# Performance work log

Measured on AMD Instinct MI355X. Metric: run time of the kernel, lower is better.

## Reference

```python
import jax, jax.numpy as jnp
import numpy as np

H = 128      # hidden_dim
D = 2        # data_dim
T = 20       # obs_len
B = 16384    # batch
PRED = 30    # pred_len
LN_EPS = 1e-5


def _lstm_cell(x, h, c, Wih, Whh, bih, bhh):
    # torch gate order: i, f, g, o
    gates = x @ Wih.T + h @ Whh.T + bih + bhh
    i, f, g, o = jnp.split(gates, 4, axis=-1)
    c = jax.nn.sigmoid(f) * c + jax.nn.sigmoid(i) * jnp.tanh(g)
    h = jax.nn.sigmoid(o) * jnp.tanh(c)
    return h, c


def _encode(seq, Wih, Whh, bih, bhh):
    # seq: [T, B, D]; return final (h, c)
    b = seq.shape[1]
    h0 = jnp.zeros((b, H), seq.dtype)
    def step(carry, x):
        h, c = _lstm_cell(x, carry[0], carry[1], Wih, Whh, bih, bhh)
        return (h, c), None
    (h, c), _ = jax.lax.scan(step, (h0, h0), seq)
    return h, c


def _layernorm(x, g, b):
    m = jnp.mean(x, axis=-1, keepdims=True)
    v = jnp.var(x, axis=-1, keepdims=True)
    return (x - m) * jax.lax.rsqrt(v + LN_EPS) * g + b


def setup_inputs() -> dict:
    key = jax.random.key(0)
    ks = jax.random.split(key, 20)
    s_in = 1.0 / np.sqrt(H)  # torch default LSTM init scale
    def W(k, shape):
        return jax.random.normal(k, shape, jnp.float32) * s_in
    return {
        "pos": jax.random.normal(ks[0], (T, B, D), jnp.float32),
        "speed": jax.random.normal(ks[1], (T, B, D), jnp.float32),
        "Wih_pe": W(ks[2], (4 * H, D)), "Whh_pe": W(ks[3], (4 * H, H)),
        "bih_pe": W(ks[4], (4 * H,)), "bhh_pe": W(ks[5], (4 * H,)),
        "Wih_se": W(ks[6], (4 * H, D)), "Whh_se": W(ks[7], (4 * H, H)),
        "bih_se": W(ks[8], (4 * H,)), "bhh_se": W(ks[9], (4 * H,)),
        "ln_g": jnp.ones((H,), jnp.float32), "ln_b": jnp.zeros((H,), jnp.float32),
        "Wih_sd": W(ks[10], (4 * H, D)), "Whh_sd": W(ks[11], (4 * H, H)),
        "bih_sd": W(ks[12], (4 * H,)), "bhh_sd": W(ks[13], (4 * H,)),
        "Wih_pd": W(ks[14], (4 * H, D)), "Whh_pd": W(ks[15], (4 * H, H)),
        "bih_pd": W(ks[16], (4 * H,)), "bhh_pd": W(ks[17], (4 * H,)),
        "Wfc": W(ks[18], (D, H)), "bfc": jnp.zeros((D,), jnp.float32),
    }


def reference(pos, speed, Wih_pe, Whh_pe, bih_pe, bhh_pe,
              Wih_se, Whh_se, bih_se, bhh_se, ln_g, ln_b,
              Wih_sd, Whh_sd, bih_sd, bhh_sd,
              Wih_pd, Whh_pd, bih_pd, bhh_pd, Wfc, bfc):
    hpo, cpo = _encode(pos, Wih_pe, Whh_pe, bih_pe, bhh_pe)
    hpo = _layernorm(hpo, ln_g, ln_b)
    cpo = _layernorm(cpo, ln_g, ln_b)
    hsp, csp = _encode(speed, Wih_se, Whh_se, bih_se, bhh_se)
    hsp = _layernorm(hsp, ln_g, ln_b)
    csp = _layernorm(csp, ln_g, ln_b)

    # concat_features=False path
    hds, cds = hpo + hsp, cpo + csp
    curr_speed, curr_pos = speed[-1], pos[-1]

    def step(carry, _):
        hds, cds, hpo, cpo, cs, cp = carry
        hds, cds = _lstm_cell(cs, hds, cds, Wih_sd, Whh_sd, bih_sd, bhh_sd)
        cs = hds @ Wfc.T + bfc
        hpo, cpo = _lstm_cell(cp, hpo, cpo, Wih_pd, Whh_pd, bih_pd, bhh_pd)
        cp = hpo @ Wfc.T + bfc
        return (hds, cds, hpo, cpo, cs, cp), (cp, cs)

    _, (pos_out, speed_out) = jax.lax.scan(
        step, (hds, cds, hpo, cpo, curr_speed, curr_pos), None, length=PRED)
    return pos_out, speed_out  # each [PRED, B, D]
```

## Files before the change

kernel.cpp:

```cpp
#include <hip/hip_runtime.h>

#define H 128
#define D 2
#define T_OBS 20
#define BATCH 16384
#define PRED 30
#define M 32
#define NTH 512
#define HP 136
#define FP 132
#define LN_EPS 1e-5f

typedef __attribute__((ext_vector_type(8))) _Float16 half8_t;
typedef __attribute__((ext_vector_type(4))) float float4_t;

__device__ __forceinline__ float fast_rcp(float x){ return __builtin_amdgcn_rcpf(x); }
__device__ __forceinline__ float sig_f(float x){ return fast_rcp(1.f + __expf(-x)); }
__device__ __forceinline__ float tanh_f(float x){ return 1.f - 2.f*fast_rcp(__expf(2.f*x)+1.f); }

struct PhaseConsts {
  half8_t bw[4][4];
  float bs[4], w0[4], w1[4];
};

__device__ __forceinline__ void load_phase(PhaseConsts& P, const float* __restrict__ Whh,
                                           const float* __restrict__ Wih,
                                           const float* __restrict__ bih,
                                           const float* __restrict__ bhh,
                                           int wv, int l15, int q){
#pragma unroll
  for(int g=0; g<4; g++){
    const int n = g*H + 16*wv + l15;
    P.bs[g] = bih[n] + bhh[n];
    P.w0[g] = Wih[n*D + 0];
    P.w1[g] = Wih[n*D + 1];
#pragma unroll
    for(int ks=0; ks<4; ks++){
      const float* p = Whh + (size_t)n*H + ks*32 + q*8;
      float4 a = *(const float4*)p;
      float4 b = *(const float4*)(p+4);
      half8_t f;
      f[0]=(_Float16)a.x; f[1]=(_Float16)a.y; f[2]=(_Float16)a.z; f[3]=(_Float16)a.w;
      f[4]=(_Float16)b.x; f[5]=(_Float16)b.y; f[6]=(_Float16)b.z; f[7]=(_Float16)b.w;
      P.bw[g][ks] = f;
    }
  }
}

__device__ __forceinline__ void load_phase_dec(PhaseConsts& P, const float* __restrict__ Whh,
                                               const float* __restrict__ Wih,
                                               const float* __restrict__ bih,
                                               const float* __restrict__ bhh,
                                               const float* __restrict__ Wfc,
                                               const float* __restrict__ bfc,
                                               int wv, int l15, int q){
#pragma unroll
  for(int g=0; g<4; g++){
    const int n = g*H + 16*wv + l15;
    const float wi0 = Wih[n*D + 0];
    const float wi1 = Wih[n*D + 1];
    P.bs[g] = bih[n] + bhh[n] + wi0*bfc[0] + wi1*bfc[1];
    P.w0[g] = wi0;
    P.w1[g] = wi1;
#pragma unroll
    for(int ks=0; ks<4; ks++){
      const float* p  = Whh + (size_t)n*H + ks*32 + q*8;
      const float* f0 = Wfc + 0*H + ks*32 + q*8;
      const float* f1 = Wfc + 1*H + ks*32 + q*8;
      half8_t f;
#pragma unroll
      for(int j=0;j<8;j++){
        f[j] = (_Float16)(p[j] + wi0*f0[j] + wi1*f1[j]);
      }
      P.bw[g][ks] = f;
    }
  }
}

template<bool HASX>
__device__ __forceinline__ void cell_step(_Float16 (*hsh)[M][HP], int cur,
                                          const float* __restrict__ xsrc,
                                          const PhaseConsts& P, float (&c)[2][4],
                                          int wv, int l15, int q){
  float4_t acc[2][4];
  if constexpr (HASX){
#pragma unroll
    for(int mh=0; mh<2; mh++){
      float x0[4], x1[4];
#pragma unroll
      for(int r=0; r<4; r++){
        x0[r] = xsrc[(mh*16 + 4*q+r)*2 + 0];
        x1[r] = xsrc[(mh*16 + 4*q+r)*2 + 1];
      }
#pragma unroll
      for(int g=0; g<4; g++)
#pragma unroll
        for(int r=0; r<4; r++)
          acc[mh][g][r] = fmaf(P.w1[g], x1[r], fmaf(P.w0[g], x0[r], P.bs[g]));
    }
  } else {
#pragma unroll
    for(int mh=0; mh<2; mh++)
#pragma unroll
      for(int g=0; g<4; g++)
#pragma unroll
        for(int r=0; r<4; r++)
          acc[mh][g][r] = P.bs[g];
  }

#pragma unroll
  for(int ks=0; ks<4; ks++){
#pragma unroll
    for(int mh=0; mh<2; mh++){
      const half8_t a = *(const half8_t*)&hsh[cur][mh*16 + l15][ks*32 + q*8];
#pragma unroll
      for(int g=0; g<4; g++){
        acc[mh][g] = __builtin_amdgcn_mfma_f32_16x16x32_f16(a, P.bw[g][ks], acc[mh][g], 0,0,0);
      }
    }
  }
  const int nxt = cur ^ 1;
  const int u = 16*wv + l15;
#pragma unroll
  for(int mh=0; mh<2; mh++){
#pragma unroll
    for(int r=0; r<4; r++){
      const float iv = sig_f(acc[mh][0][r]);
      const float fv = sig_f(acc[mh][1][r]);
      const float gv = tanh_f(acc[mh][2][r]);
      const float ov = sig_f(acc[mh][3][r]);
      const float cc = fmaf(fv, c[mh][r], iv*gv);
      c[mh][r] = cc;
      const float hv = ov * tanh_f(cc);
      const int m = mh*16 + 4*q + r;
      hsh[nxt][m][u] = (_Float16)hv;
    }
  }
  __syncthreads();
}

__device__ __forceinline__ void layernorm32(const float (*src)[FP], float (*dst)[FP],
                                            const float* __restrict__ g,
                                            const float* __restrict__ b, int tid){
  const int m = tid >> 4, sub = tid & 15;
  float v[8];
  float s = 0.f, s2 = 0.f;
#pragma unroll
  for(int j=0;j<8;j++){ v[j] = src[m][sub*8+j]; s += v[j]; s2 = fmaf(v[j], v[j], s2); }
#pragma unroll
  for(int msk=1; msk<16; msk<<=1){ s += __shfl_xor(s, msk, 64); s2 += __shfl_xor(s2, msk, 64); }
  const float mean = s * (1.f/H);
  const float var  = s2 * (1.f/H) - mean*mean;
  const float inv  = rsqrtf(var + LN_EPS);
#pragma unroll
  for(int j=0;j<8;j++){
    const int u = sub*8+j;
    dst[m][u] = fmaf((v[j]-mean)*inv, g[u], b[u]);
  }
}

__device__ __forceinline__ void fc_out(const _Float16 (*hb)[HP], const float (*wfc)[H],
                                       const float* __restrict__ bfcs,
                                       float* __restrict__ gout, int row0, int tid){
  const int m = tid >> 4, d = (tid >> 3) & 1, ch = tid & 7;
  const _Float16* hp = &hb[m][ch*16];
  float s = 0.f;
#pragma unroll
  for(int j=0;j<16;j++) s = fmaf((float)hp[j], wfc[d][ch*16+j], s);
  s += __shfl_xor(s, 1, 64); s += __shfl_xor(s, 2, 64); s += __shfl_xor(s, 4, 64);
  if(ch == 0){
    gout[(size_t)(row0+m)*D + d] = s + bfcs[d];
  }
}

__device__ __forceinline__ void fc_delta(const _Float16 (*hb)[HP], const float (*wfc)[H],
                                         const float* __restrict__ bfcs,
                                         const float* __restrict__ xlast,
                                         float (*xb)[D], int tid){
  const int m = tid >> 4, d = (tid >> 3) & 1, ch = tid & 7;
  const _Float16* hp = &hb[m][ch*16];
  float s = 0.f;
#pragma unroll
  for(int j=0;j<16;j++) s = fmaf((float)hp[j], wfc[d][ch*16+j], s);
  s += __shfl_xor(s, 1, 64); s += __shfl_xor(s, 2, 64); s += __shfl_xor(s, 4, 64);
  if(ch == 0){
    xb[m][d] = xlast[m*D + d] - (s + bfcs[d]);
  }
}

__global__ __launch_bounds__(NTH, 2) void traj_kernel(
    const float* __restrict__ pos, const float* __restrict__ speed,
    const float* __restrict__ Wih_pe, const float* __restrict__ Whh_pe,
    const float* __restrict__ bih_pe, const float* __restrict__ bhh_pe,
    const float* __restrict__ Wih_se, const float* __restrict__ Whh_se,
    const float* __restrict__ bih_se, const float* __restrict__ bhh_se,
    const float* __restrict__ ln_g, const float* __restrict__ ln_b,
    const float* __restrict__ Wih_sd, const float* __restrict__ Whh_sd,
    const float* __restrict__ bih_sd, const float* __restrict__ bhh_sd,
    const float* __restrict__ Wih_pd, const float* __restrict__ Whh_pd,
    const float* __restrict__ bih_pd, const float* __restrict__ bhh_pd,
    const float* __restrict__ Wfc, const float* __restrict__ bfc,
    float* __restrict__ out)
{
  __shared__ __align__(16) _Float16 hsh[2][M][HP];
  __shared__ float tmpf[M][FP];
  __shared__ float hpoN[M][FP];
  __shared__ float cpoN[M][FP];
  __shared__ float seqx[2][T_OBS][M][D];
  __shared__ float xbuf[M][D];
  __shared__ float wfcs[D][H];
  __shared__ float bfcs[2];

  const int tid  = threadIdx.x;
  const int lane = tid & 63;
  const int wv   = tid >> 6;
  const int q    = lane >> 4;
  const int l15  = lane & 15;
  const int row0 = blockIdx.x * M;
  const int u    = 16*wv + l15;

  for(int idx = tid; idx < 2*T_OBS*M*D; idx += NTH){
    const int chain = idx / (T_OBS*M*D);
    const int rem   = idx % (T_OBS*M*D);
    const int t = rem / (M*D), e = rem % (M*D);
    const float* src = chain ? speed : pos;
    seqx[chain][t][e>>1][e&1] = src[(size_t)t*BATCH*D + row0*D + e];
  }
  if(tid < D*H) wfcs[tid>>7][tid&127] = Wfc[tid];
  if(tid < 2)   bfcs[tid] = bfc[tid];
  { int* hz = (int*)&hsh[0][0][0];
    for(int idx = tid; idx < M*HP/2; idx += NTH) hz[idx] = 0; }

  PhaseConsts P;
  float c[2][4];
  load_phase(P, Whh_pe, Wih_pe, bih_pe, bhh_pe, wv, l15, q);
#pragma unroll
  for(int mh=0;mh<2;mh++)
#pragma unroll
    for(int r=0;r<4;r++) c[mh][r] = 0.f;
  __syncthreads();

  int cur = 0;
  for(int t=0; t<T_OBS; t++){ cell_step<true>(hsh, cur, &seqx[0][t][0][0], P, c, wv, l15, q); cur ^= 1; }
  for(int idx=tid; idx<M*H; idx+=NTH){
    const int m = idx>>7, uu = idx&127;
    tmpf[m][uu] = (float)hsh[cur][m][uu];
  }
  __syncthreads();
  layernorm32(tmpf, hpoN, ln_g, ln_b, tid);
  __syncthreads();
#pragma unroll
  for(int mh=0;mh<2;mh++)
#pragma unroll
    for(int r=0;r<4;r++) tmpf[mh*16 + 4*q+r][u] = c[mh][r];
  __syncthreads();
  layernorm32(tmpf, cpoN, ln_g, ln_b, tid);
  __syncthreads();

  load_phase(P, Whh_se, Wih_se, bih_se, bhh_se, wv, l15, q);
#pragma unroll
  for(int mh=0;mh<2;mh++)
#pragma unroll
    for(int r=0;r<4;r++) c[mh][r] = 0.f;
  for(int idx=tid; idx<M*H; idx+=NTH){
    const int m = idx>>7, uu = idx&127;
    hsh[0][m][uu] = (_Float16)0.f;
  }
  cur = 0;
  __syncthreads();
  for(int t=0; t<T_OBS; t++){ cell_step<true>(hsh, cur, &seqx[1][t][0][0], P, c, wv, l15, q); cur ^= 1; }
  for(int idx=tid; idx<M*H; idx+=NTH){
    const int m = idx>>7, uu = idx&127;
    tmpf[m][uu] = (float)hsh[cur][m][uu];
  }
  __syncthreads();
  layernorm32(tmpf, tmpf, ln_g, ln_b, tid);
  __syncthreads();
  for(int idx=tid; idx<M*H; idx+=NTH){
    const int m = idx>>7, uu = idx&127;
    hsh[0][m][uu] = (_Float16)(tmpf[m][uu] + hpoN[m][uu]);
  }
  __syncthreads();
#pragma unroll
  for(int mh=0;mh<2;mh++)
#pragma unroll
    for(int r=0;r<4;r++) tmpf[mh*16 + 4*q+r][u] = c[mh][r];
  __syncthreads();
  layernorm32(tmpf, tmpf, ln_g, ln_b, tid);
  __syncthreads();
#pragma unroll
  for(int mh=0;mh<2;mh++)
#pragma unroll
    for(int r=0;r<4;r++) c[mh][r] = tmpf[mh*16 + 4*q+r][u] + cpoN[mh*16 + 4*q+r][u];

  load_phase_dec(P, Whh_sd, Wih_sd, bih_sd, bhh_sd, Wfc, bfc, wv, l15, q);
  fc_delta(hsh[0], wfcs, bfcs, &seqx[1][T_OBS-1][0][0], xbuf, tid);
  __syncthreads();

  float* spd_out = out + (size_t)PRED*BATCH*D;
  cur = 0;
  cell_step<true>(hsh, cur, &xbuf[0][0], P, c, wv, l15, q);
  fc_out(hsh[cur^1], wfcs, bfcs, spd_out, row0, tid);
  cur ^= 1;
  for(int t=1; t<PRED; t++){
    cell_step<false>(hsh, cur, nullptr, P, c, wv, l15, q);
    fc_out(hsh[cur^1], wfcs, bfcs, spd_out + (size_t)t*BATCH*D, row0, tid);
    cur ^= 1;
  }
  __syncthreads();

  for(int idx=tid; idx<M*H; idx+=NTH){
    const int m = idx>>7, uu = idx&127;
    hsh[0][m][uu] = (_Float16)hpoN[m][uu];
  }
#pragma unroll
  for(int mh=0;mh<2;mh++)
#pragma unroll
    for(int r=0;r<4;r++) c[mh][r] = cpoN[mh*16 + 4*q+r][u];
  load_phase_dec(P, Whh_pd, Wih_pd, bih_pd, bhh_pd, Wfc, bfc, wv, l15, q);
  __syncthreads();
  fc_delta(hsh[0], wfcs, bfcs, &seqx[0][T_OBS-1][0][0], xbuf, tid);
  __syncthreads();

  cur = 0;
  cell_step<true>(hsh, cur, &xbuf[0][0], P, c, wv, l15, q);
  fc_out(hsh[cur^1], wfcs, bfcs, out, row0, tid);
  cur ^= 1;
  for(int t=1; t<PRED; t++){
    cell_step<false>(hsh, cur, nullptr, P, c, wv, l15, q);
    fc_out(hsh[cur^1], wfcs, bfcs, out + (size_t)t*BATCH*D, row0, tid);
    cur ^= 1;
  }
}

extern "C" void kernel_launch(void* const* d_in, const int* in_sizes, int n_in,
                              void* d_out, int out_size, void* d_ws, size_t ws_size,
                              hipStream_t stream)
{
  const float* pos    = (const float*)d_in[0];
  const float* speed  = (const float*)d_in[1];
  const float* Wih_pe = (const float*)d_in[2];
  const float* Whh_pe = (const float*)d_in[3];
  const float* bih_pe = (const float*)d_in[4];
  const float* bhh_pe = (const float*)d_in[5];
  const float* Wih_se = (const float*)d_in[6];
  const float* Whh_se = (const float*)d_in[7];
  const float* bih_se = (const float*)d_in[8];
  const float* bhh_se = (const float*)d_in[9];
  const float* ln_g   = (const float*)d_in[10];
  const float* ln_b   = (const float*)d_in[11];
  const float* Wih_sd = (const float*)d_in[12];
  const float* Whh_sd = (const float*)d_in[13];
  const float* bih_sd = (const float*)d_in[14];
  const float* bhh_sd = (const float*)d_in[15];
  const float* Wih_pd = (const float*)d_in[16];
  const float* Whh_pd = (const float*)d_in[17];
  const float* bih_pd = (const float*)d_in[18];
  const float* bhh_pd = (const float*)d_in[19];
  const float* Wfc    = (const float*)d_in[20];
  const float* bfc    = (const float*)d_in[21];

  traj_kernel<<<BATCH/M, NTH, 0, stream>>>(
      pos, speed, Wih_pe, Whh_pe, bih_pe, bhh_pe,
      Wih_se, Whh_se, bih_se, bhh_se, ln_g, ln_b,
      Wih_sd, Whh_sd, bih_sd, bhh_sd, Wih_pd, Whh_pd, bih_pd, bhh_pd,
      Wfc, bfc, (float*)d_out);
}
```

Before: 547.5 us.

## Split batch rows across two wave groups with 1024-thread blocks

Doubles the block to 1024 threads. Each group of 8 waves now handles one 16-row half of the 32-row tile instead of one wave handling both halves. This halves the MFMA and gate work per wave on each recurrent step, shortening the serial critical path between barriers. LayerNorm and FC helpers are gated to the first 512 threads. The cost is a heavier __syncthreads across 16 waves, half the threads idle during FC, and the loss of the 2-blocks-per-CU launch bound, which may cut occupancy.

```diff
diff --git a/kernel.cpp b/kernel.cpp
--- a/kernel.cpp
+++ b/kernel.cpp
@@ -6,7 +6,7 @@
 #define BATCH 16384
 #define PRED 30
 #define M 32
-#define NTH 512
+#define NTH 1024
 #define HP 136
 #define FP 132
 #define LN_EPS 1e-5f
@@ -27,10 +27,10 @@
                                            const float* __restrict__ Wih,
                                            const float* __restrict__ bih,
                                            const float* __restrict__ bhh,
-                                           int wv, int l15, int q){
+                                           int wvu, int l15, int q){
 #pragma unroll
   for(int g=0; g<4; g++){
-    const int n = g*H + 16*wv + l15;
+    const int n = g*H + 16*wvu + l15;
     P.bs[g] = bih[n] + bhh[n];
     P.w0[g] = Wih[n*D + 0];
     P.w1[g] = Wih[n*D + 1];
@@ -53,10 +53,10 @@
                                                const float* __restrict__ bhh,
                                                const float* __restrict__ Wfc,
                                                const float* __restrict__ bfc,
-                                               int wv, int l15, int q){
+                                               int wvu, int l15, int q){
 #pragma unroll
   for(int g=0; g<4; g++){
-    const int n = g*H + 16*wv + l15;
+    const int n = g*H + 16*wvu + l15;
     const float wi0 = Wih[n*D + 0];
     const float wi1 = Wih[n*D + 1];
     P.bs[g] = bih[n] + bhh[n] + wi0*bfc[0] + wi1*bfc[1];
@@ -80,61 +80,48 @@
 template<bool HASX>
 __device__ __forceinline__ void cell_step(_Float16 (*hsh)[M][HP], int cur,
                                           const float* __restrict__ xsrc,
-                                          const PhaseConsts& P, float (&c)[2][4],
-                                          int wv, int l15, int q){
-  float4_t acc[2][4];
+                                          const PhaseConsts& P, float (&c)[4],
+                                          int mrow0, int arow, int u, int l15, int q){
+  float4_t acc[4];
   if constexpr (HASX){
-#pragma unroll
-    for(int mh=0; mh<2; mh++){
-      float x0[4], x1[4];
-#pragma unroll
-      for(int r=0; r<4; r++){
-        x0[r] = xsrc[(mh*16 + 4*q+r)*2 + 0];
-        x1[r] = xsrc[(mh*16 + 4*q+r)*2 + 1];
-      }
-#pragma unroll
-      for(int g=0; g<4; g++)
-#pragma unroll
-        for(int r=0; r<4; r++)
-          acc[mh][g][r] = fmaf(P.w1[g], x1[r], fmaf(P.w0[g], x0[r], P.bs[g]));
+    float x0[4], x1[4];
+#pragma unroll
+    for(int r=0; r<4; r++){
+      x0[r] = xsrc[(mrow0 + 4*q+r)*2 + 0];
+      x1[r] = xsrc[(mrow0 + 4*q+r)*2 + 1];
     }
+#pragma unroll
+    for(int g=0; g<4; g++)
+#pragma unroll
+      for(int r=0; r<4; r++)
+        acc[g][r] = fmaf(P.w1[g], x1[r], fmaf(P.w0[g], x0[r], P.bs[g]));
   } else {
 #pragma unroll
-    for(int mh=0; mh<2; mh++)
-#pragma unroll
-      for(int g=0; g<4; g++)
-#pragma unroll
-        for(int r=0; r<4; r++)
-          acc[mh][g][r] = P.bs[g];
+    for(int g=0; g<4; g++)
+#pragma unroll
+      for(int r=0; r<4; r++)
+        acc[g][r] = P.bs[g];
   }
 
 #pragma unroll
   for(int ks=0; ks<4; ks++){
-#pragma unroll
-    for(int mh=0; mh<2; mh++){
-      const half8_t a = *(const half8_t*)&hsh[cur][mh*16 + l15][ks*32 + q*8];
-#pragma unroll
-      for(int g=0; g<4; g++){
-        acc[mh][g] = __builtin_amdgcn_mfma_f32_16x16x32_f16(a, P.bw[g][ks], acc[mh][g], 0,0,0);
-      }
+    const half8_t a = *(const half8_t*)&hsh[cur][arow][ks*32 + q*8];
+#pragma unroll
+    for(int g=0; g<4; g++){
+      acc[g] = __builtin_amdgcn_mfma_f32_16x16x32_f16(a, P.bw[g][ks], acc[g], 0,0,0);
     }
   }
   const int nxt = cur ^ 1;
-  const int u = 16*wv + l15;
-#pragma unroll
-  for(int mh=0; mh<2; mh++){
-#pragma unroll
-    for(int r=0; r<4; r++){
-      const float iv = sig_f(acc[mh][0][r]);
-      const float fv = sig_f(acc[mh][1][r]);
-      const float gv = tanh_f(acc[mh][2][r]);
-      const float ov = sig_f(acc[mh][3][r]);
-      const float cc = fmaf(fv, c[mh][r], iv*gv);
-      c[mh][r] = cc;
-      const float hv = ov * tanh_f(cc);
-      const int m = mh*16 + 4*q + r;
-      hsh[nxt][m][u] = (_Float16)hv;
-    }
+#pragma unroll
+  for(int r=0; r<4; r++){
+    const float iv = sig_f(acc[0][r]);
+    const float fv = sig_f(acc[1][r]);
+    const float gv = tanh_f(acc[2][r]);
+    const float ov = sig_f(acc[3][r]);
+    const float cc = fmaf(fv, c[r], iv*gv);
+    c[r] = cc;
+    const float hv = ov * tanh_f(cc);
+    hsh[nxt][mrow0 + 4*q + r][u] = (_Float16)hv;
   }
   __syncthreads();
 }
@@ -142,6 +129,7 @@
 __device__ __forceinline__ void layernorm32(const float (*src)[FP], float (*dst)[FP],
                                             const float* __restrict__ g,
                                             const float* __restrict__ b, int tid){
+  if(tid >= 512) return;
   const int m = tid >> 4, sub = tid & 15;
   float v[8];
   float s = 0.f, s2 = 0.f;
@@ -162,6 +150,7 @@
 __device__ __forceinline__ void fc_out(const _Float16 (*hb)[HP], const float (*wfc)[H],
                                        const float* __restrict__ bfcs,
                                        float* __restrict__ gout, int row0, int tid){
+  if(tid >= 512) return;
   const int m = tid >> 4, d = (tid >> 3) & 1, ch = tid & 7;
   const _Float16* hp = &hb[m][ch*16];
   float s = 0.f;
@@ -177,6 +166,7 @@
                                          const float* __restrict__ bfcs,
                                          const float* __restrict__ xlast,
                                          float (*xb)[D], int tid){
+  if(tid >= 512) return;
   const int m = tid >> 4, d = (tid >> 3) & 1, ch = tid & 7;
   const _Float16* hp = &hb[m][ch*16];
   float s = 0.f;
@@ -188,7 +178,7 @@
   }
 }
 
-__global__ __launch_bounds__(NTH, 2) void traj_kernel(
+__global__ __launch_bounds__(NTH) void traj_kernel(
     const float* __restrict__ pos, const float* __restrict__ speed,
     const float* __restrict__ Wih_pe, const float* __restrict__ Whh_pe,
     const float* __restrict__ bih_pe, const float* __restrict__ bhh_pe,
@@ -214,10 +204,14 @@
   const int tid  = threadIdx.x;
   const int lane = tid & 63;
   const int wv   = tid >> 6;
+  const int wvu  = wv & 7;
+  const int mh   = wv >> 3;
   const int q    = lane >> 4;
   const int l15  = lane & 15;
   const int row0 = blockIdx.x * M;
-  const int u    = 16*wv + l15;
+  const int u    = 16*wvu + l15;
+  const int mrow0= mh*16;
+  const int arow = mrow0 + l15;
 
   for(int idx = tid; idx < 2*T_OBS*M*D; idx += NTH){
     const int chain = idx / (T_OBS*M*D);
@@ -232,16 +226,14 @@
     for(int idx = tid; idx < M*HP/2; idx += NTH) hz[idx] = 0; }
 
   PhaseConsts P;
-  float c[2][4];
-  load_phase(P, Whh_pe, Wih_pe, bih_pe, bhh_pe, wv, l15, q);
-#pragma unroll
-  for(int mh=0;mh<2;mh++)
-#pragma unroll
-    for(int r=0;r<4;r++) c[mh][r] = 0.f;
+  float c[4];
+  load_phase(P, Whh_pe, Wih_pe, bih_pe, bhh_pe, wvu, l15, q);
+#pragma unroll
+  for(int r=0;r<4;r++) c[r] = 0.f;
   __syncthreads();
 
   int cur = 0;
-  for(int t=0; t<T_OBS; t++){ cell_step<true>(hsh, cur, &seqx[0][t][0][0], P, c, wv, l15, q); cur ^= 1; }
+  for(int t=0; t<T_OBS; t++){ cell_step<true>(hsh, cur, &seqx[0][t][0][0], P, c, mrow0, arow, u, l15, q); cur ^= 1; }
   for(int idx=tid; idx<M*H; idx+=NTH){
     const int m = idx>>7, uu = idx&127;
     tmpf[m][uu] = (float)hsh[cur][m][uu];
@@ -250,25 +242,21 @@
   layernorm32(tmpf, hpoN, ln_g, ln_b, tid);
   __syncthreads();
 #pragma unroll
-  for(int mh=0;mh<2;mh++)
-#pragma unroll
-    for(int r=0;r<4;r++) tmpf[mh*16 + 4*q+r][u] = c[mh][r];
+  for(int r=0;r<4;r++) tmpf[mrow0 + 4*q+r][u] = c[r];
   __syncthreads();
   layernorm32(tmpf, cpoN, ln_g, ln_b, tid);
   __syncthreads();
 
-  load_phase(P, Whh_se, Wih_se, bih_se, bhh_se, wv, l15, q);
-#pragma unroll
-  for(int mh=0;mh<2;mh++)
-#pragma unroll
-    for(int r=0;r<4;r++) c[mh][r] = 0.f;
+  load_phase(P, Whh_se, Wih_se, bih_se, bhh_se, wvu, l15, q);
+#pragma unroll
+  for(int r=0;r<4;r++) c[r] = 0.f;
   for(int idx=tid; idx<M*H; idx+=NTH){
     const int m = idx>>7, uu = idx&127;
     hsh[0][m][uu] = (_Float16)0.f;
   }
   cur = 0;
   __syncthreads();
-  for(int t=0; t<T_OBS; t++){ cell_step<true>(hsh, cur, &seqx[1][t][0][0], P, c, wv, l15, q); cur ^= 1; }
+  for(int t=0; t<T_OBS; t++){ cell_step<true>(hsh, cur, &seqx[1][t][0][0], P, c, mrow0, arow, u, l15, q); cur ^= 1; }
   for(int idx=tid; idx<M*H; idx+=NTH){
     const int m = idx>>7, uu = idx&127;
     tmpf[m][uu] = (float)hsh[cur][m][uu];
@@ -282,28 +270,24 @@
   }
   __syncthreads();
 #pragma unroll
-  for(int mh=0;mh<2;mh++)
-#pragma unroll
-    for(int r=0;r<4;r++) tmpf[mh*16 + 4*q+r][u] = c[mh][r];
+  for(int r=0;r<4;r++) tmpf[mrow0 + 4*q+r][u] = c[r];
   __syncthreads();
   layernorm32(tmpf, tmpf, ln_g, ln_b, tid);
   __syncthreads();
 #pragma unroll
-  for(int mh=0;mh<2;mh++)
-#pragma unroll
-    for(int r=0;r<4;r++) c[mh][r] = tmpf[mh*16 + 4*q+r][u] + cpoN[mh*16 + 4*q+r][u];
-
-  load_phase_dec(P, Whh_sd, Wih_sd, bih_sd, bhh_sd, Wfc, bfc, wv, l15, q);
+  for(int r=0;r<4;r++) c[r] = tmpf[mrow0 + 4*q+r][u] + cpoN[mrow0 + 4*q+r][u];
+
+  load_phase_dec(P, Whh_sd, Wih_sd, bih_sd, bhh_sd, Wfc, bfc, wvu, l15, q);
   fc_delta(hsh[0], wfcs, bfcs, &seqx[1][T_OBS-1][0][0], xbuf, tid);
   __syncthreads();
 
   float* spd_out = out + (size_t)PRED*BATCH*D;
   cur = 0;
-  cell_step<true>(hsh, cur, &xbuf[0][0], P, c, wv, l15, q);
+  cell_step<true>(hsh, cur, &xbuf[0][0], P, c, mrow0, arow, u, l15, q);
   fc_out(hsh[cur^1], wfcs, bfcs, spd_out, row0, tid);
   cur ^= 1;
   for(int t=1; t<PRED; t++){
-    cell_step<false>(hsh, cur, nullptr, P, c, wv, l15, q);
+    cell_step<false>(hsh, cur, nullptr, P, c, mrow0, arow, u, l15, q);
     fc_out(hsh[cur^1], wfcs, bfcs, spd_out + (size_t)t*BATCH*D, row0, tid);
     cur ^= 1;
   }
@@ -314,20 +298,18 @@
     hsh[0][m][uu] = (_Float16)hpoN[m][uu];
   }
 #pragma unroll
-  for(int mh=0;mh<2;mh++)
-#pragma unroll
-    for(int r=0;r<4;r++) c[mh][r] = cpoN[mh*16 + 4*q+r][u];
-  load_phase_dec(P, Whh_pd, Wih_pd, bih_pd, bhh_pd, Wfc, bfc, wv, l15, q);
+  for(int r=0;r<4;r++) c[r] = cpoN[mrow0 + 4*q+r][u];
+  load_phase_dec(P, Whh_pd, Wih_pd, bih_pd, bhh_pd, Wfc, bfc, wvu, l15, q);
   __syncthreads();
   fc_delta(hsh[0], wfcs, bfcs, &seqx[0][T_OBS-1][0][0], xbuf, tid);
   __syncthreads();
 
   cur = 0;
-  cell_step<true>(hsh, cur, &xbuf[0][0], P, c, wv, l15, q);
+  cell_step<true>(hsh, cur, &xbuf[0][0], P, c, mrow0, arow, u, l15, q);
   fc_out(hsh[cur^1], wfcs, bfcs, out, row0, tid);
   cur ^= 1;
   for(int t=1; t<PRED; t++){
-    cell_step<false>(hsh, cur, nullptr, P, c, wv, l15, q);
+    cell_step<false>(hsh, cur, nullptr, P, c, mrow0, arow, u, l15, q);
     fc_out(hsh[cur^1], wfcs, bfcs, out + (size_t)t*BATCH*D, row0, tid);
     cur ^= 1;
   }
```

After: 0.9998 ms. 82.6% more time.

## Interleave the two independent LSTM chains in one fused dual-cell step

Applied to the files above, without the earlier changes.

The pos and speed encoders run together in one loop, and so do the two decoders, rather than one after the other. Each step issues MFMAs for both chains between barriers, which halves the number of sequential steps and __syncthreads, and gives the scheduler independent work to hide MFMA and transcendental latency. The cost is double the register state (two PhaseConsts with fp16 weight fragments plus two accumulator sets) and double the shared h buffer, which risks spills or lower occupancy under launch_bounds(512,2). Several expressions are also rewritten as fmaf.

```diff
diff --git a/kernel.cpp b/kernel.cpp
--- a/kernel.cpp
+++ b/kernel.cpp
@@ -16,7 +16,7 @@
 
 __device__ __forceinline__ float fast_rcp(float x){ return __builtin_amdgcn_rcpf(x); }
 __device__ __forceinline__ float sig_f(float x){ return fast_rcp(1.f + __expf(-x)); }
-__device__ __forceinline__ float tanh_f(float x){ return 1.f - 2.f*fast_rcp(__expf(2.f*x)+1.f); }
+__device__ __forceinline__ float tanh_f(float x){ return fmaf(-2.f, fast_rcp(__expf(2.f*x)+1.f), 1.f); }
 
 struct PhaseConsts {
   half8_t bw[4][4];
@@ -59,7 +59,7 @@
     const int n = g*H + 16*wv + l15;
     const float wi0 = Wih[n*D + 0];
     const float wi1 = Wih[n*D + 1];
-    P.bs[g] = bih[n] + bhh[n] + wi0*bfc[0] + wi1*bfc[1];
+    P.bs[g] = fmaf(wi1, bfc[1], fmaf(wi0, bfc[0], bih[n] + bhh[n]));
     P.w0[g] = wi0;
     P.w1[g] = wi1;
 #pragma unroll
@@ -70,7 +70,7 @@
       half8_t f;
 #pragma unroll
       for(int j=0;j<8;j++){
-        f[j] = (_Float16)(p[j] + wi0*f0[j] + wi1*f1[j]);
+        f[j] = (_Float16)fmaf(wi1, f1[j], fmaf(wi0, f0[j], p[j]));
       }
       P.bw[g][ks] = f;
     }
@@ -78,25 +78,41 @@
 }
 
 template<bool HASX>
-__device__ __forceinline__ void cell_step(_Float16 (*hsh)[M][HP], int cur,
-                                          const float* __restrict__ xsrc,
-                                          const PhaseConsts& P, float (&c)[2][4],
+__device__ __forceinline__ void cell_dual(_Float16 (*hsh)[2][M][HP], int cur,
+                                          const float* __restrict__ xs0,
+                                          const float* __restrict__ xs1,
+                                          const PhaseConsts& Pa, const PhaseConsts& Pb,
+                                          float (&ca)[2][4], float (&cb)[2][4],
                                           int wv, int l15, int q){
-  float4_t acc[2][4];
+  float4_t aa[2][4], ab[2][4];
   if constexpr (HASX){
 #pragma unroll
     for(int mh=0; mh<2; mh++){
       float x0[4], x1[4];
 #pragma unroll
       for(int r=0; r<4; r++){
-        x0[r] = xsrc[(mh*16 + 4*q+r)*2 + 0];
-        x1[r] = xsrc[(mh*16 + 4*q+r)*2 + 1];
+        x0[r] = xs0[(mh*16 + 4*q+r)*2 + 0];
+        x1[r] = xs0[(mh*16 + 4*q+r)*2 + 1];
       }
 #pragma unroll
       for(int g=0; g<4; g++)
 #pragma unroll
         for(int r=0; r<4; r++)
-          acc[mh][g][r] = fmaf(P.w1[g], x1[r], fmaf(P.w0[g], x0[r], P.bs[g]));
+          aa[mh][g][r] = fmaf(Pa.w1[g], x1[r], fmaf(Pa.w0[g], x0[r], Pa.bs[g]));
+    }
+#pragma unroll
+    for(int mh=0; mh<2; mh++){
+      float x0[4], x1[4];
+#pragma unroll
+      for(int r=0; r<4; r++){
+        x0[r] = xs1[(mh*16 + 4*q+r)*2 + 0];
+        x1[r] = xs1[(mh*16 + 4*q+r)*2 + 1];
+      }
+#pragma unroll
+      for(int g=0; g<4; g++)
+#pragma unroll
+        for(int r=0; r<4; r++)
+          ab[mh][g][r] = fmaf(Pb.w1[g], x1[r], fmaf(Pb.w0[g], x0[r], Pb.bs[g]));
     }
   } else {
 #pragma unroll
@@ -104,19 +120,24 @@
 #pragma unroll
       for(int g=0; g<4; g++)
 #pragma unroll
-        for(int r=0; r<4; r++)
-          acc[mh][g][r] = P.bs[g];
+        for(int r=0; r<4; r++){
+          aa[mh][g][r] = Pa.bs[g];
+          ab[mh][g][r] = Pb.bs[g];
+        }
   }
 
 #pragma unroll
   for(int ks=0; ks<4; ks++){
 #pragma unroll
     for(int mh=0; mh<2; mh++){
-      const half8_t a = *(const half8_t*)&hsh[cur][mh*16 + l15][ks*32 + q*8];
-#pragma unroll
-      for(int g=0; g<4; g++){
-        acc[mh][g] = __builtin_amdgcn_mfma_f32_16x16x32_f16(a, P.bw[g][ks], acc[mh][g], 0,0,0);
-      }
+      const half8_t h0 = *(const half8_t*)&hsh[cur][0][mh*16 + l15][ks*32 + q*8];
+#pragma unroll
+      for(int g=0; g<4; g++)
+        aa[mh][g] = __builtin_amdgcn_mfma_f32_16x16x32_f16(h0, Pa.bw[g][ks], aa[mh][g], 0,0,0);
+      const half8_t h1 = *(const half8_t*)&hsh[cur][1][mh*16 + l15][ks*32 + q*8];
+#pragma unroll
+      for(int g=0; g<4; g++)
+        ab[mh][g] = __builtin_amdgcn_mfma_f32_16x16x32_f16(h1, Pb.bw[g][ks], ab[mh][g], 0,0,0);
     }
   }
   const int nxt = cur ^ 1;
@@ -125,15 +146,25 @@
   for(int mh=0; mh<2; mh++){
 #pragma unroll
     for(int r=0; r<4; r++){
-      const float iv = sig_f(acc[mh][0][r]);
-      const float fv = sig_f(acc[mh][1][r]);
-      const float gv = tanh_f(acc[mh][2][r]);
-      const float ov = sig_f(acc[mh][3][r]);
-      const float cc = fmaf(fv, c[mh][r], iv*gv);
-      c[mh][r] = cc;
-      const float hv = ov * tanh_f(cc);
       const int m = mh*16 + 4*q + r;
-      hsh[nxt][m][u] = (_Float16)hv;
+      {
+        const float iv = sig_f(aa[mh][0][r]);
+        const float fv = sig_f(aa[mh][1][r]);
+        const float gv = tanh_f(aa[mh][2][r]);
+        const float ov = sig_f(aa[mh][3][r]);
+        const float cc = fmaf(fv, ca[mh][r], iv*gv);
+        ca[mh][r] = cc;
+        hsh[nxt][0][m][u] = (_Float16)(ov * tanh_f(cc));
+      }
+      {
+        const float iv = sig_f(ab[mh][0][r]);
+        const float fv = sig_f(ab[mh][1][r]);
+        const float gv = tanh_f(ab[mh][2][r]);
+        const float ov = sig_f(ab[mh][3][r]);
+        const float cc = fmaf(fv, cb[mh][r], iv*gv);
+        cb[mh][r] = cc;
+        hsh[nxt][1][m][u] = (_Float16)(ov * tanh_f(cc));
+      }
     }
   }
   __syncthreads();
@@ -150,7 +181,7 @@
 #pragma unroll
   for(int msk=1; msk<16; msk<<=1){ s += __shfl_xor(s, msk, 64); s2 += __shfl_xor(s2, msk, 64); }
   const float mean = s * (1.f/H);
-  const float var  = s2 * (1.f/H) - mean*mean;
+  const float var  = fmaf(-mean, mean, s2 * (1.f/H));
   const float inv  = rsqrtf(var + LN_EPS);
 #pragma unroll
   for(int j=0;j<8;j++){
@@ -159,32 +190,42 @@
   }
 }
 
-__device__ __forceinline__ void fc_out(const _Float16 (*hb)[HP], const float (*wfc)[H],
-                                       const float* __restrict__ bfcs,
-                                       float* __restrict__ gout, int row0, int tid){
-  const int m = tid >> 4, d = (tid >> 3) & 1, ch = tid & 7;
-  const _Float16* hp = &hb[m][ch*16];
-  float s = 0.f;
-#pragma unroll
-  for(int j=0;j<16;j++) s = fmaf((float)hp[j], wfc[d][ch*16+j], s);
-  s += __shfl_xor(s, 1, 64); s += __shfl_xor(s, 2, 64); s += __shfl_xor(s, 4, 64);
-  if(ch == 0){
-    gout[(size_t)(row0+m)*D + d] = s + bfcs[d];
-  }
-}
-
-__device__ __forceinline__ void fc_delta(const _Float16 (*hb)[HP], const float (*wfc)[H],
-                                         const float* __restrict__ bfcs,
-                                         const float* __restrict__ xlast,
-                                         float (*xb)[D], int tid){
-  const int m = tid >> 4, d = (tid >> 3) & 1, ch = tid & 7;
-  const _Float16* hp = &hb[m][ch*16];
-  float s = 0.f;
-#pragma unroll
-  for(int j=0;j<16;j++) s = fmaf((float)hp[j], wfc[d][ch*16+j], s);
-  s += __shfl_xor(s, 1, 64); s += __shfl_xor(s, 2, 64); s += __shfl_xor(s, 4, 64);
-  if(ch == 0){
-    xb[m][d] = xlast[m*D + d] - (s + bfcs[d]);
+__device__ __forceinline__ void fc_out_dual(const _Float16 (*hb)[M][HP], const float (*wfc)[H],
+                                            const float* __restrict__ bfcs,
+                                            float* __restrict__ g0, float* __restrict__ g1,
+                                            int row0, int tid){
+  const int m = tid >> 4, d = (tid >> 3) & 1, cn = tid & 7;
+#pragma unroll
+  for(int ch=0; ch<2; ch++){
+    const _Float16* hp = &hb[ch][m][cn*16];
+    float s = 0.f;
+#pragma unroll
+    for(int j=0;j<16;j++) s = fmaf((float)hp[j], wfc[d][cn*16+j], s);
+    s += __shfl_xor(s, 1, 64); s += __shfl_xor(s, 2, 64); s += __shfl_xor(s, 4, 64);
+    if(cn == 0){
+      float* g = ch ? g1 : g0;
+      g[(size_t)(row0+m)*D + d] = s + bfcs[d];
+    }
+  }
+}
+
+__device__ __forceinline__ void fc_delta_dual(const _Float16 (*hb)[M][HP], const float (*wfc)[H],
+                                              const float* __restrict__ bfcs,
+                                              const float* __restrict__ xl0,
+                                              const float* __restrict__ xl1,
+                                              float (*xb)[M][D], int tid){
+  const int m = tid >> 4, d = (tid >> 3) & 1, cn = tid & 7;
+#pragma unroll
+  for(int ch=0; ch<2; ch++){
+    const _Float16* hp = &hb[ch][m][cn*16];
+    float s = 0.f;
+#pragma unroll
+    for(int j=0;j<16;j++) s = fmaf((float)hp[j], wfc[d][cn*16+j], s);
+    s += __shfl_xor(s, 1, 64); s += __shfl_xor(s, 2, 64); s += __shfl_xor(s, 4, 64);
+    if(cn == 0){
+      const float* xl = ch ? xl1 : xl0;
+      xb[ch][m][d] = xl[m*D + d] - (s + bfcs[d]);
+    }
   }
 }
 
@@ -202,12 +243,12 @@
     const float* __restrict__ Wfc, const float* __restrict__ bfc,
     float* __restrict__ out)
 {
-  __shared__ __align__(16) _Float16 hsh[2][M][HP];
+  __shared__ __align__(16) _Float16 hsh[2][2][M][HP];
   __shared__ float tmpf[M][FP];
   __shared__ float hpoN[M][FP];
   __shared__ float cpoN[M][FP];
   __shared__ float seqx[2][T_OBS][M][D];
-  __shared__ float xbuf[M][D];
+  __shared__ float xbuf[2][M][D];
   __shared__ float wfcs[D][H];
   __shared__ float bfcs[2];
 
@@ -228,107 +269,81 @@
   }
   if(tid < D*H) wfcs[tid>>7][tid&127] = Wfc[tid];
   if(tid < 2)   bfcs[tid] = bfc[tid];
-  { int* hz = (int*)&hsh[0][0][0];
-    for(int idx = tid; idx < M*HP/2; idx += NTH) hz[idx] = 0; }
-
-  PhaseConsts P;
-  float c[2][4];
-  load_phase(P, Whh_pe, Wih_pe, bih_pe, bhh_pe, wv, l15, q);
+  { int* hz = (int*)&hsh[0][0][0][0];
+    for(int idx = tid; idx < M*HP; idx += NTH) hz[idx] = 0; }
+
+  PhaseConsts Pa, Pb;
+  float ca[2][4], cb[2][4];
+  load_phase(Pa, Whh_pe, Wih_pe, bih_pe, bhh_pe, wv, l15, q);
+  load_phase(Pb, Whh_se, Wih_se, bih_se, bhh_se, wv, l15, q);
 #pragma unroll
   for(int mh=0;mh<2;mh++)
 #pragma unroll
-    for(int r=0;r<4;r++) c[mh][r] = 0.f;
+    for(int r=0;r<4;r++){ ca[mh][r] = 0.f; cb[mh][r] = 0.f; }
   __syncthreads();
 
   int cur = 0;
-  for(int t=0; t<T_OBS; t++){ cell_step<true>(hsh, cur, &seqx[0][t][0][0], P, c, wv, l15, q); cur ^= 1; }
+  for(int t=0; t<T_OBS; t++){
+    cell_dual<true>(hsh, cur, &seqx[0][t][0][0], &seqx[1][t][0][0], Pa, Pb, ca, cb, wv, l15, q);
+    cur ^= 1;
+  }
   for(int idx=tid; idx<M*H; idx+=NTH){
     const int m = idx>>7, uu = idx&127;
-    tmpf[m][uu] = (float)hsh[cur][m][uu];
+    tmpf[m][uu] = (float)hsh[cur][0][m][uu];
   }
   __syncthreads();
   layernorm32(tmpf, hpoN, ln_g, ln_b, tid);
   __syncthreads();
-#pragma unroll
-  for(int mh=0;mh<2;mh++)
-#pragma unroll
-    for(int r=0;r<4;r++) tmpf[mh*16 + 4*q+r][u] = c[mh][r];
-  __syncthreads();
-  layernorm32(tmpf, cpoN, ln_g, ln_b, tid);
-  __syncthreads();
-
-  load_phase(P, Whh_se, Wih_se, bih_se, bhh_se, wv, l15, q);
-#pragma unroll
-  for(int mh=0;mh<2;mh++)
-#pragma unroll
-    for(int r=0;r<4;r++) c[mh][r] = 0.f;
   for(int idx=tid; idx<M*H; idx+=NTH){
     const int m = idx>>7, uu = idx&127;
-    hsh[0][m][uu] = (_Float16)0.f;
-  }
-  cur = 0;
-  __syncthreads();
-  for(int t=0; t<T_OBS; t++){ cell_step<true>(hsh, cur, &seqx[1][t][0][0], P, c, wv, l15, q); cur ^= 1; }
+    tmpf[m][uu] = (float)hsh[cur][1][m][uu];
+  }
+  __syncthreads();
+  layernorm32(tmpf, tmpf, ln_g, ln_b, tid);
+  __syncthreads();
   for(int idx=tid; idx<M*H; idx+=NTH){
     const int m = idx>>7, uu = idx&127;
-    tmpf[m][uu] = (float)hsh[cur][m][uu];
-  }
+    hsh[0][0][m][uu] = (_Float16)(tmpf[m][uu] + hpoN[m][uu]);
+    hsh[0][1][m][uu] = (_Float16)hpoN[m][uu];
+  }
+  __syncthreads();
+#pragma unroll
+  for(int mh=0;mh<2;mh++)
+#pragma unroll
+    for(int r=0;r<4;r++) tmpf[mh*16 + 4*q+r][u] = ca[mh][r];
+  __syncthreads();
+  layernorm32(tmpf, cpoN, ln_g, ln_b, tid);
+  __syncthreads();
+#pragma unroll
+  for(int mh=0;mh<2;mh++)
+#pragma unroll
+    for(int r=0;r<4;r++) tmpf[mh*16 + 4*q+r][u] = cb[mh][r];
   __syncthreads();
   layernorm32(tmpf, tmpf, ln_g, ln_b, tid);
   __syncthreads();
-  for(int idx=tid; idx<M*H; idx+=NTH){
-    const int m = idx>>7, uu = idx&127;
-    hsh[0][m][uu] = (_Float16)(tmpf[m][uu] + hpoN[m][uu]);
-  }
-  __syncthreads();
 #pragma unroll
   for(int mh=0;mh<2;mh++)
 #pragma unroll
-    for(int r=0;r<4;r++) tmpf[mh*16 + 4*q+r][u] = c[mh][r];
-  __syncthreads();
-  layernorm32(tmpf, tmpf, ln_g, ln_b, tid);
-  __syncthreads();
-#pragma unroll
-  for(int mh=0;mh<2;mh++)
-#pragma unroll
-    for(int r=0;r<4;r++) c[mh][r] = tmpf[mh*16 + 4*q+r][u] + cpoN[mh*16 + 4*q+r][u];
-
-  load_phase_dec(P, Whh_sd, Wih_sd, bih_sd, bhh_sd, Wfc, bfc, wv, l15, q);
-  fc_delta(hsh[0], wfcs, bfcs, &seqx[1][T_OBS-1][0][0], xbuf, tid);
+    for(int r=0;r<4;r++){
+      const int m = mh*16 + 4*q + r;
+      ca[mh][r] = tmpf[m][u] + cpoN[m][u];
+      cb[mh][r] = cpoN[m][u];
+    }
+
+  load_phase_dec(Pa, Whh_sd, Wih_sd, bih_sd, bhh_sd, Wfc, bfc, wv, l15, q);
+  load_phase_dec(Pb, Whh_pd, Wih_pd, bih_pd, bhh_pd, Wfc, bfc, wv, l15, q);
+  fc_delta_dual(hsh[0], wfcs, bfcs, &seqx[1][T_OBS-1][0][0], &seqx[0][T_OBS-1][0][0], xbuf, tid);
   __syncthreads();
 
   float* spd_out = out + (size_t)PRED*BATCH*D;
   cur = 0;
-  cell_step<true>(hsh, cur, &xbuf[0][0], P, c, wv, l15, q);
-  fc_out(hsh[cur^1], wfcs, bfcs, spd_out, row0, tid);
+  cell_dual<true>(hsh, cur, &xbuf[0][0][0], &xbuf[1][0][0], Pa, Pb, ca, cb, wv, l15, q);
+  fc_out_dual(hsh[cur^1], wfcs, bfcs, spd_out, out, row0, tid);
   cur ^= 1;
   for(int t=1; t<PRED; t++){
-    cell_step<false>(hsh, cur, nullptr, P, c, wv, l15, q);
-    fc_out(hsh[cur^1], wfcs, bfcs, spd_out + (size_t)t*BATCH*D, row0, tid);
-    cur ^= 1;
-  }
-  __syncthreads();
-
-  for(int idx=tid; idx<M*H; idx+=NTH){
-    const int m = idx>>7, uu = idx&127;
-    hsh[0][m][uu] = (_Float16)hpoN[m][uu];
-  }
-#pragma unroll
-  for(int mh=0;mh<2;mh++)
-#pragma unroll
-    for(int r=0;r<4;r++) c[mh][r] = cpoN[mh*16 + 4*q+r][u];
-  load_phase_dec(P, Whh_pd, Wih_pd, bih_pd, bhh_pd, Wfc, bfc, wv, l15, q);
-  __syncthreads();
-  fc_delta(hsh[0], wfcs, bfcs, &seqx[0][T_OBS-1][0][0], xbuf, tid);
-  __syncthreads();
-
-  cur = 0;
-  cell_step<true>(hsh, cur, &xbuf[0][0], P, c, wv, l15, q);
-  fc_out(hsh[cur^1], wfcs, bfcs, out, row0, tid);
-  cur ^= 1;
-  for(int t=1; t<PRED; t++){
-    cell_step<false>(hsh, cur, nullptr, P, c, wv, l15, q);
-    fc_out(hsh[cur^1], wfcs, bfcs, out + (size_t)t*BATCH*D, row0, tid);
+    cell_dual<false>(hsh, cur, nullptr, nullptr, Pa, Pb, ca, cb, wv, l15, q);
+    fc_out_dual(hsh[cur^1], wfcs, bfcs,
+                spd_out + (size_t)t*BATCH*D, out + (size_t)t*BATCH*D, row0, tid);
     cur ^= 1;
   }
 }
```

After: 826.1 us. 50.9% more time.
